# Optimization experiments

Hardware: AMD Instinct MI355X
Metric: run time of the kernel (lower is better)

The kernel has to match this reference:

```python
import math
import jax, jax.numpy as jnp
import numpy as np

G, PQ, PV = 12, 4, 8

def setup_inputs() -> dict:
    key = jax.random.key(0)
    ks = jax.random.split(key, 14)
    N, L, Cn, Ce, Ch = 1, 512, 384, 128, 192
    Node = jax.random.normal(ks[0], (N, L, Cn), jnp.float32)
    Edge = jax.random.normal(ks[1], (N, L, L, Ce), jnp.float32)
    # proper rotation matrices via QR of random gaussians
    raw = jax.random.normal(ks[2], (N, L, 3, 3), jnp.float32)
    rots, _ = jnp.linalg.qr(raw)
    trans = jax.random.normal(ks[3], (N, L, 3), jnp.float32) * 10.0
    def lin(k, fan_in, fan_out):
        return jax.random.normal(k, (fan_in, fan_out), jnp.float32) / np.sqrt(fan_in)
    return {
        'Node': Node, 'Edge': Edge, 'rots': rots, 'trans': trans,
        'Wq': lin(ks[4], Cn, Ch), 'Wk': lin(ks[5], Cn, Ch), 'Wv': lin(ks[6], Cn, Ch),
        'Wqv': lin(ks[7], Cn, 3 * G * PQ), 'Wkv': lin(ks[8], Cn, 3 * G * PQ),
        'Wvv': lin(ks[9], Cn, 3 * G * PV), 'Wbias': lin(ks[10], Ce, G),
        'gamma': jnp.zeros((G,), jnp.float32),
        'Wout': lin(ks[11], Ce * G + Ch + G * PV * 4, Cn),
        'bout': jnp.zeros((Cn,), jnp.float32),
    }

def reference(Node, Edge, rots, trans, Wq, Wk, Wv, Wqv, Wkv, Wvv, Wbias, gamma, Wout, bout):
    N, L, Cn = Node.shape
    Ce = Edge.shape[-1]
    Ch = Wq.shape[1]
    ppg = Ch // G
    t = trans / 10.0  # Frame(T.rots, T.trans / 10.0)
    q = (Node @ Wq).reshape(N, L, G, ppg)
    k = (Node @ Wk).reshape(N, L, G, ppg)
    v = (Node @ Wv).reshape(N, L, G, ppg)
    qv = (Node @ Wqv).reshape(N, L, G, PQ, 3)
    kv = (Node @ Wkv).reshape(N, L, G, PQ, 3)
    vv = (Node @ Wvv).reshape(N, L, G, PV, 3)
    apply_frame = lambda p: jnp.einsum('nlij,nlgpj->nlgpi', rots, p) + t[:, :, None, None]
    qv = apply_frame(qv)
    kv = apply_frame(kv)
    vv = apply_frame(vv)
    # pairwise squared point distances, summed over xyz and query points -> [N,L,L,G]
    d = qv[:, :, None] - kv[:, None]
    sq = jnp.sum(d * d, axis=(-1, -2))
    bias = jnp.einsum('nijc,cg->nijg', Edge, Wbias)
    WC = math.sqrt(2.0 / 9.0 / PQ)
    WL = math.sqrt(1.0 / 3.0)
    attn = jnp.einsum('nlgc,nmgc->nlmg', q, k) / math.sqrt(ppg) + bias
    attn = attn - jax.nn.softplus(gamma) * (WC / 2.0) * sq
    attn = jax.nn.softmax(WL * attn, axis=2)  # softmax over key index m
    O_Edge = jnp.einsum('nijg,nijc->nigc', attn, Edge).reshape(N, L, G * Ce)
    O_Node = jnp.einsum('nijg,njgc->nigc', attn, v).reshape(N, L, Ch)
    O_vec = jnp.einsum('nijg,njgpc->nigpc', attn, vv)
    # invert_apply: R^T (x - t)
    O_vec = jnp.einsum('nlji,nlgpj->nlgpi', rots, O_vec - t[:, :, None, None])
    O_norm = jnp.sqrt(jnp.sum(O_vec * O_vec, axis=-1) + 1e-8).reshape(N, L, -1)
    O_vec = O_vec.reshape(N, L, -1)
    feat = jnp.concatenate([O_Edge, O_Node, O_vec, O_norm], axis=-1)
    return feat @ Wout + bout
```

## Files before the change

kernel.cpp:

```cpp
#include <hip/hip_runtime.h>
#include <math.h>

#define LQ 512
#define CN 384
#define CE 128
#define CH 192
#define NG 12
#define PPG 16
#define FEAT 2112
#define NPROJ 1152

#define WS_RAW  0u
#define WS_QVG  589824u
#define WS_KVT  663552u
#define WS_VVG  737280u
#define WS_QN   884736u
#define WS_KNT  890880u
#define WS_KT   897024u
#define WS_ATT  995328u
#define WS_FEAT 4141056u
#define WS_PART 5222400u
#define WS_PM   WS_PART
#define WS_PS   (WS_PART + 12288u)

__global__ __launch_bounds__(256) void k1a_gemm(
    const float* __restrict__ Node,
    const float* __restrict__ Wq, const float* __restrict__ Wk,
    const float* __restrict__ Wv, const float* __restrict__ Wqv,
    const float* __restrict__ Wkv, const float* __restrict__ Wvv,
    float* __restrict__ ws)
{
    __shared__ float As[64][68];
    __shared__ float Bs[64][48];
    const int tid = threadIdx.x;
    const int cb = blockIdx.x % 24;
    const int l0 = (blockIdx.x / 24) * 64;
    const int col0 = cb * 48;

    const float* W; int nc, lc0;
    if (col0 < 192)      { W = Wq;  nc = 192; lc0 = col0; }
    else if (col0 < 384) { W = Wk;  nc = 192; lc0 = col0 - 192; }
    else if (col0 < 576) { W = Wv;  nc = 192; lc0 = col0 - 384; }
    else if (col0 < 720) { W = Wqv; nc = 144; lc0 = col0 - 576; }
    else if (col0 < 864) { W = Wkv; nc = 144; lc0 = col0 - 720; }
    else                 { W = Wvv; nc = 288; lc0 = col0 - 864; }

    const int tx = tid & 15, ty = tid >> 4;
    float acc[4][3];
#pragma unroll
    for (int r = 0; r < 4; ++r)
#pragma unroll
        for (int c = 0; c < 3; ++c) acc[r][c] = 0.f;

    for (int kc = 0; kc < 6; ++kc) {
        __syncthreads();
#pragma unroll
        for (int pass = 0; pass < 4; ++pass) {
            int m = (tid >> 4) + pass * 16;
            int kk = (tid & 15) * 4;
            const float4 a = *(const float4*)(Node + (size_t)(l0 + m) * CN + kc * 64 + kk);
            As[kk + 0][m] = a.x; As[kk + 1][m] = a.y;
            As[kk + 2][m] = a.z; As[kk + 3][m] = a.w;
        }
#pragma unroll
        for (int p = 0; p < 12; ++p) {
            int idx = p * 256 + tid;
            int kk = idx / 48, c = idx - kk * 48;
            Bs[kk][c] = W[(size_t)(kc * 64 + kk) * nc + lc0 + c];
        }
        __syncthreads();
#pragma unroll 8
        for (int kk = 0; kk < 64; ++kk) {
            const float4 av = *(const float4*)&As[kk][tx * 4];
            const float b0 = Bs[kk][ty * 3 + 0];
            const float b1 = Bs[kk][ty * 3 + 1];
            const float b2 = Bs[kk][ty * 3 + 2];
            acc[0][0] = fmaf(av.x, b0, acc[0][0]); acc[0][1] = fmaf(av.x, b1, acc[0][1]); acc[0][2] = fmaf(av.x, b2, acc[0][2]);
            acc[1][0] = fmaf(av.y, b0, acc[1][0]); acc[1][1] = fmaf(av.y, b1, acc[1][1]); acc[1][2] = fmaf(av.y, b2, acc[1][2]);
            acc[2][0] = fmaf(av.z, b0, acc[2][0]); acc[2][1] = fmaf(av.z, b1, acc[2][1]); acc[2][2] = fmaf(av.z, b2, acc[2][2]);
            acc[3][0] = fmaf(av.w, b0, acc[3][0]); acc[3][1] = fmaf(av.w, b1, acc[3][1]); acc[3][2] = fmaf(av.w, b2, acc[3][2]);
        }
    }
    float* raw = ws + WS_RAW;
#pragma unroll
    for (int r = 0; r < 4; ++r)
#pragma unroll
        for (int c = 0; c < 3; ++c)
            raw[(size_t)(l0 + tx * 4 + r) * NPROJ + col0 + ty * 3 + c] = acc[r][c];
    if (col0 >= 192 && col0 < 384) {
#pragma unroll
        for (int r = 0; r < 4; ++r)
#pragma unroll
            for (int c = 0; c < 3; ++c)
                ws[WS_KT + (size_t)(col0 - 192 + ty * 3 + c) * LQ + l0 + tx * 4 + r] = acc[r][c];
    }
}

__global__ __launch_bounds__(256) void k1b_vec(
    const float* __restrict__ rots, const float* __restrict__ trans,
    float* __restrict__ ws)
{
    __shared__ float sqbuf[96];
    const int tid = threadIdx.x;
    const int l = blockIdx.x;
    const float* raw = ws + WS_RAW + (size_t)l * NPROJ;

    if (tid < 192) {
        int src, pt, typ;
        if (tid < 48)      { typ = 0; pt = tid;      src = 576 + pt * 3; }
        else if (tid < 96) { typ = 1; pt = tid - 48; src = 720 + pt * 3; }
        else               { typ = 2; pt = tid - 96; src = 864 + pt * 3; }
        float v0 = raw[src], v1 = raw[src + 1], v2 = raw[src + 2];
        const float* R = rots + l * 9;
        float o0 = R[0] * v0 + R[1] * v1 + R[2] * v2 + trans[l * 3 + 0] * 0.1f;
        float o1 = R[3] * v0 + R[4] * v1 + R[5] * v2 + trans[l * 3 + 1] * 0.1f;
        float o2 = R[6] * v0 + R[7] * v1 + R[8] * v2 + trans[l * 3 + 2] * 0.1f;
        if (typ == 0) {
            float* dst = ws + WS_QVG + (size_t)l * 144 + pt * 3;
            dst[0] = o0; dst[1] = o1; dst[2] = o2;
        } else if (typ == 1) {
            ws[WS_KVT + (size_t)(pt * 3 + 0) * LQ + l] = o0;
            ws[WS_KVT + (size_t)(pt * 3 + 1) * LQ + l] = o1;
            ws[WS_KVT + (size_t)(pt * 3 + 2) * LQ + l] = o2;
        } else {
            float* dst = ws + WS_VVG + (size_t)l * 288 + pt * 3;
            dst[0] = o0; dst[1] = o1; dst[2] = o2;
        }
        if (tid < 96) sqbuf[tid] = o0 * o0 + o1 * o1 + o2 * o2;
    }
    __syncthreads();
    if (tid < 24) {
        int typ = tid / 12, g = tid % 12;
        int b = typ * 48 + g * 4;
        float s = sqbuf[b] + sqbuf[b + 1] + sqbuf[b + 2] + sqbuf[b + 3];
        if (typ == 0) ws[WS_QN + (size_t)l * 12 + g] = s;
        else          ws[WS_KNT + (size_t)g * LQ + l] = s;
    }
}

__global__ __launch_bounds__(256, 4) void k2_attn(
    const float* __restrict__ Edge, const float* __restrict__ Wbias,
    const float* __restrict__ gamma, float* __restrict__ ws)
{
    __shared__ float et[256 * 33];
    __shared__ float cgls[NG];
    __shared__ float red[4][NG];
    const int tid = threadIdx.x;
    const int i = blockIdx.x >> 1;
    const int h = blockIdx.x & 1;
    const int j = h * 256 + tid;

    if (tid < NG)
        cgls[tid] = log1pf(__expf(gamma[tid])) * 0.11785113019775793f;
    __syncthreads();

    float lgs[NG];
    {
        const float* qrow  = ws + WS_RAW + (size_t)i * NPROJ;
        const float* qvrow = ws + WS_QVG + (size_t)i * 144;
        const float* qnrow = ws + WS_QN  + (size_t)i * NG;
        const float* KT  = ws + WS_KT;
        const float* KVT = ws + WS_KVT;
        const float* KNT = ws + WS_KNT;
#pragma unroll
        for (int g = 0; g < NG; ++g) {
            float qk = 0.f;
#pragma unroll
            for (int u = 0; u < PPG; ++u)
                qk = fmaf(qrow[g * PPG + u], KT[(size_t)(g * PPG + u) * LQ + j], qk);
            float dt = 0.f;
#pragma unroll
            for (int u = 0; u < 12; ++u)
                dt = fmaf(qvrow[g * 12 + u], KVT[(size_t)(g * 12 + u) * LQ + j], dt);
            float sq = qnrow[g] + KNT[(size_t)g * LQ + j] - 2.f * dt;
            lgs[g] = qk * 0.25f - cgls[g] * sq;
        }
    }

    const float4* e4 = (const float4*)Edge + ((size_t)i * LQ + h * 256) * 32;
    for (int ch = 0; ch < 4; ++ch) {
        __syncthreads();
#pragma unroll
        for (int kk = 0; kk < 8; ++kk) {
            int idx = kk * 256 + tid;
            int jr = idx >> 3, c4 = idx & 7;
            float4 v = e4[(size_t)jr * 32 + ch * 8 + c4];
            float* d = et + jr * 33 + c4 * 4;
            d[0] = v.x; d[1] = v.y; d[2] = v.z; d[3] = v.w;
        }
        __syncthreads();
        const float* wbch = Wbias + ch * 32 * NG;
        const float* r0 = et + tid * 33;
#pragma unroll 4
        for (int c = 0; c < 32; ++c) {
            float e0 = r0[c];
            const float* wb = wbch + c * NG;
#pragma unroll
            for (int g = 0; g < NG; ++g) lgs[g] = fmaf(e0, wb[g], lgs[g]);
        }
    }

    const float WL = 0.5773502691896258f;
    const int wid = tid >> 6, lane = tid & 63;
    float pm[NG];
#pragma unroll
    for (int g = 0; g < NG; ++g) pm[g] = lgs[g];
#pragma unroll
    for (int g = 0; g < NG; ++g)
        for (int off = 1; off < 64; off <<= 1)
            pm[g] = fmaxf(pm[g], __shfl_xor(pm[g], off));
    if (lane == 0) {
#pragma unroll
        for (int g = 0; g < NG; ++g) red[wid][g] = pm[g];
    }
    __syncthreads();
    float gm[NG];
#pragma unroll
    for (int g = 0; g < NG; ++g)
        gm[g] = fmaxf(fmaxf(red[0][g], red[1][g]), fmaxf(red[2][g], red[3][g]));
    if (tid < NG)
        ws[WS_PM + ((size_t)i * 2 + h) * NG + tid] =
            fmaxf(fmaxf(red[0][tid], red[1][tid]), fmaxf(red[2][tid], red[3][tid]));
    __syncthreads();

    float ps[NG];
#pragma unroll
    for (int g = 0; g < NG; ++g) {
        float e = __expf(WL * (lgs[g] - gm[g]));
        lgs[g] = e;
        ps[g] = e;
    }
#pragma unroll
    for (int g = 0; g < NG; ++g)
        for (int off = 1; off < 64; off <<= 1)
            ps[g] += __shfl_xor(ps[g], off);
    if (lane == 0) {
#pragma unroll
        for (int g = 0; g < NG; ++g) red[wid][g] = ps[g];
    }
    __syncthreads();
    if (tid < NG)
        ws[WS_PS + ((size_t)i * 2 + h) * NG + tid] =
            red[0][tid] + red[1][tid] + red[2][tid] + red[3][tid];

    float4* dst = (float4*)(ws + WS_ATT + ((size_t)i * LQ + j) * NG);
    float4 s0, s1, s2;
    s0.x = lgs[0]; s0.y = lgs[1]; s0.z = lgs[2];  s0.w = lgs[3];
    s1.x = lgs[4]; s1.y = lgs[5]; s1.z = lgs[6];  s1.w = lgs[7];
    s2.x = lgs[8]; s2.y = lgs[9]; s2.z = lgs[10]; s2.w = lgs[11];
    dst[0] = s0; dst[1] = s1; dst[2] = s2;
}

__global__ __launch_bounds__(256) void k3_out(
    const float* __restrict__ Edge, const float* __restrict__ rots,
    const float* __restrict__ trans, float* __restrict__ ws)
{
    __shared__ float at[LQ][13];
    __shared__ float bufA[4][32][NG][4];
    __shared__ float ovec[288];
    __shared__ float sc[2][NG];
    const int tid = threadIdx.x;
    const int qi = blockIdx.x;
    const float* att = ws + WS_ATT + (size_t)qi * LQ * NG;

    if (tid < 24) {
        const float WL = 0.5773502691896258f;
        int hh = tid / NG, g = tid % NG;
        float m0 = ws[WS_PM + ((size_t)qi * 2 + 0) * NG + g];
        float m1 = ws[WS_PM + ((size_t)qi * 2 + 1) * NG + g];
        float ss0 = ws[WS_PS + ((size_t)qi * 2 + 0) * NG + g];
        float ss1 = ws[WS_PS + ((size_t)qi * 2 + 1) * NG + g];
        float m = fmaxf(m0, m1);
        float e0 = __expf(WL * (m0 - m));
        float e1 = __expf(WL * (m1 - m));
        float denom = ss0 * e0 + ss1 * e1;
        sc[hh][g] = (hh ? e1 : e0) / denom;
    }
    __syncthreads();

    for (int m = 0; m < 2; ++m) {
        int j = tid + m * 256;
        int hh = j >> 8;
        const float4* src = (const float4*)(att + (size_t)j * NG);
        float4 a = src[0], b = src[1], c = src[2];
        at[j][0] = a.x * sc[hh][0]; at[j][1] = a.y * sc[hh][1];
        at[j][2] = a.z * sc[hh][2]; at[j][3] = a.w * sc[hh][3];
        at[j][4] = b.x * sc[hh][4]; at[j][5] = b.y * sc[hh][5];
        at[j][6] = b.z * sc[hh][6]; at[j][7] = b.w * sc[hh][7];
        at[j][8] = c.x * sc[hh][8]; at[j][9] = c.y * sc[hh][9];
        at[j][10] = c.z * sc[hh][10]; at[j][11] = c.w * sc[hh][11];
    }
    __syncthreads();

    const int w = tid >> 6, lane = tid & 63, jh = lane >> 5, c4 = lane & 31;
    float acc[NG][4];
#pragma unroll
    for (int g = 0; g < NG; ++g)
#pragma unroll
        for (int r = 0; r < 4; ++r) acc[g][r] = 0.f;
    const float4* e4 = (const float4*)(Edge + (size_t)qi * LQ * CE);
    for (int jj = 0; jj < 64; ++jj) {
        int j = w * 128 + jh * 64 + jj;
        float4 e = e4[(size_t)j * 32 + c4];
#pragma unroll
        for (int g = 0; g < NG; ++g) {
            float a = at[j][g];
            acc[g][0] = fmaf(a, e.x, acc[g][0]);
            acc[g][1] = fmaf(a, e.y, acc[g][1]);
            acc[g][2] = fmaf(a, e.z, acc[g][2]);
            acc[g][3] = fmaf(a, e.w, acc[g][3]);
        }
    }
#pragma unroll
    for (int g = 0; g < NG; ++g)
#pragma unroll
        for (int r = 0; r < 4; ++r) acc[g][r] += __shfl_xor(acc[g][r], 32);
    if (jh == 0) {
#pragma unroll
        for (int g = 0; g < NG; ++g)
#pragma unroll
            for (int r = 0; r < 4; ++r) bufA[w][c4][g][r] = acc[g][r];
    }
    __syncthreads();
    float* feat = ws + WS_FEAT + (size_t)qi * FEAT;
    for (int m = 0; m < 6; ++m) {
        int o = tid + m * 256;
        int g = o >> 7, c = o & 127;
        int cc4 = c >> 2, r = c & 3;
        feat[o] = bufA[0][cc4][g][r] + bufA[1][cc4][g][r] +
                  bufA[2][cc4][g][r] + bufA[3][cc4][g][r];
    }

    const float* raw = ws + WS_RAW;
    const float* vvg = ws + WS_VVG;
    for (int ph = 0; ph < 2; ++ph) {
        int task = tid + ph * 256;
        if (task < 192) {
            int g = task >> 4;
            float s = 0.f;
            for (int j = 0; j < LQ; ++j) s = fmaf(at[j][g], raw[(size_t)j * NPROJ + 384 + task], s);
            feat[1536 + task] = s;
        } else if (task < 480) {
            int u = task - 192;
            int g = u / 24;
            float s = 0.f;
            for (int j = 0; j < LQ; ++j) s = fmaf(at[j][g], vvg[(size_t)j * 288 + u], s);
            ovec[u] = s;
        }
    }
    __syncthreads();

    if (tid < 96) {
        int g = tid >> 3, p = tid & 7;
        const float* R = rots + qi * 9;
        float t0 = trans[qi * 3 + 0] * 0.1f;
        float t1 = trans[qi * 3 + 1] * 0.1f;
        float t2 = trans[qi * 3 + 2] * 0.1f;
        float d0 = ovec[g * 24 + p * 3 + 0] - t0;
        float d1 = ovec[g * 24 + p * 3 + 1] - t1;
        float d2 = ovec[g * 24 + p * 3 + 2] - t2;
        float o0 = R[0] * d0 + R[3] * d1 + R[6] * d2;
        float o1 = R[1] * d0 + R[4] * d1 + R[7] * d2;
        float o2 = R[2] * d0 + R[5] * d1 + R[8] * d2;
        feat[1728 + g * 24 + p * 3 + 0] = o0;
        feat[1728 + g * 24 + p * 3 + 1] = o1;
        feat[1728 + g * 24 + p * 3 + 2] = o2;
        feat[2016 + g * 8 + p] = sqrtf(o0 * o0 + o1 * o1 + o2 * o2 + 1e-8f);
    }
}

__global__ __launch_bounds__(256) void k4_gemm(const float* __restrict__ Wout,
                                               float* __restrict__ ws)
{
    __shared__ float As[64][68];
    __shared__ float Bs[64][48];
    const int tid = threadIdx.x;
    const int cc = blockIdx.x >> 6;
    const int t  = blockIdx.x & 63;
    const int l0 = (t >> 3) * 64;
    const int col0 = (t & 7) * 48;
    const float* feat = ws + WS_FEAT;

    const int tx = tid & 15, ty = tid >> 4;
    float acc[4][3];
#pragma unroll
    for (int r = 0; r < 4; ++r)
#pragma unroll
        for (int c = 0; c < 3; ++c) acc[r][c] = 0.f;

    for (int kc = cc * 11; kc < cc * 11 + 11; ++kc) {
        __syncthreads();
#pragma unroll
        for (int pass = 0; pass < 4; ++pass) {
            int m = (tid >> 4) + pass * 16;
            int kk = (tid & 15) * 4;
            const float4 a = *(const float4*)(feat + (size_t)(l0 + m) * FEAT + kc * 64 + kk);
            As[kk + 0][m] = a.x; As[kk + 1][m] = a.y;
            As[kk + 2][m] = a.z; As[kk + 3][m] = a.w;
        }
#pragma unroll
        for (int p = 0; p < 12; ++p) {
            int idx = p * 256 + tid;
            int kk = idx / 48, c = idx - kk * 48;
            Bs[kk][c] = Wout[(size_t)(kc * 64 + kk) * CN + col0 + c];
        }
        __syncthreads();
#pragma unroll 8
        for (int kk = 0; kk < 64; ++kk) {
            const float4 av = *(const float4*)&As[kk][tx * 4];
            const float b0 = Bs[kk][ty * 3 + 0];
            const float b1 = Bs[kk][ty * 3 + 1];
            const float b2 = Bs[kk][ty * 3 + 2];
            acc[0][0] = fmaf(av.x, b0, acc[0][0]); acc[0][1] = fmaf(av.x, b1, acc[0][1]); acc[0][2] = fmaf(av.x, b2, acc[0][2]);
            acc[1][0] = fmaf(av.y, b0, acc[1][0]); acc[1][1] = fmaf(av.y, b1, acc[1][1]); acc[1][2] = fmaf(av.y, b2, acc[1][2]);
            acc[2][0] = fmaf(av.z, b0, acc[2][0]); acc[2][1] = fmaf(av.z, b1, acc[2][1]); acc[2][2] = fmaf(av.z, b2, acc[2][2]);
            acc[3][0] = fmaf(av.w, b0, acc[3][0]); acc[3][1] = fmaf(av.w, b1, acc[3][1]); acc[3][2] = fmaf(av.w, b2, acc[3][2]);
        }
    }
    float* part = ws + WS_PART + (size_t)cc * LQ * CN;
#pragma unroll
    for (int r = 0; r < 4; ++r)
#pragma unroll
        for (int c = 0; c < 3; ++c)
            part[(size_t)(l0 + tx * 4 + r) * CN + col0 + ty * 3 + c] = acc[r][c];
}

__global__ __launch_bounds__(384) void k5_red(const float* __restrict__ bout,
                                              const float* __restrict__ wsc,
                                              float* __restrict__ out)
{
    const int i = blockIdx.x, n = threadIdx.x;
    const float* part = wsc + WS_PART;
    size_t idx = (size_t)i * CN + n;
    size_t st = (size_t)LQ * CN;
    out[idx] = part[idx] + part[st + idx] + part[2 * st + idx] + bout[n];
}

extern "C" void kernel_launch(void* const* d_in, const int* in_sizes, int n_in,
                              void* d_out, int out_size, void* d_ws, size_t ws_size,
                              hipStream_t stream) {
    const float* Node  = (const float*)d_in[0];
    const float* Edge  = (const float*)d_in[1];
    const float* rots  = (const float*)d_in[2];
    const float* trans = (const float*)d_in[3];
    const float* Wq    = (const float*)d_in[4];
    const float* Wk    = (const float*)d_in[5];
    const float* Wv    = (const float*)d_in[6];
    const float* Wqv   = (const float*)d_in[7];
    const float* Wkv   = (const float*)d_in[8];
    const float* Wvv   = (const float*)d_in[9];
    const float* Wbias = (const float*)d_in[10];
    const float* gamma = (const float*)d_in[11];
    const float* Wout  = (const float*)d_in[12];
    const float* bout  = (const float*)d_in[13];
    float* ws = (float*)d_ws;

    k1a_gemm<<<192, 256, 0, stream>>>(Node, Wq, Wk, Wv, Wqv, Wkv, Wvv, ws);
    k1b_vec<<<512, 256, 0, stream>>>(rots, trans, ws);
    k2_attn<<<1024, 256, 0, stream>>>(Edge, Wbias, gamma, ws);
    k3_out<<<512, 256, 0, stream>>>(Edge, rots, trans, ws);
    k4_gemm<<<192, 256, 0, stream>>>(Wout, ws);
    k5_red<<<512, 384, 0, stream>>>(bout, ws, (float*)d_out);
}
```

Measured before the change: 202.0 us.

## Fuse attention-weighted Edge reduction into attention kernel to avoid second Edge read

Computes per-half partial O_Edge sums inside k2 using the unnormalized exponentials kept in shared memory, and stores them to workspace. k3 then combines the two halves with the softmax rescale factors instead of rereading Edge. This removes a second full pass over the large Edge tensor. In exchange k2 uses more shared memory, lowers its occupancy bound, and re-streams Edge chunks through shared memory.

```diff
diff --git a/kernel.cpp b/kernel.cpp
--- a/kernel.cpp
+++ b/kernel.cpp
@@ -22,6 +22,7 @@
 #define WS_PART 5222400u
 #define WS_PM   WS_PART
 #define WS_PS   (WS_PART + 12288u)
+#define WS_OEP  5812224u
 
 __global__ __launch_bounds__(256) void k1a_gemm(
     const float* __restrict__ Node,
@@ -138,11 +139,12 @@
     }
 }
 
-__global__ __launch_bounds__(256, 4) void k2_attn(
+__global__ __launch_bounds__(256, 3) void k2_attn(
     const float* __restrict__ Edge, const float* __restrict__ Wbias,
     const float* __restrict__ gamma, float* __restrict__ ws)
 {
     __shared__ float et[256 * 33];
+    __shared__ float exl[256 * 13];
     __shared__ float cgls[NG];
     __shared__ float red[4][NG];
     const int tid = threadIdx.x;
@@ -229,6 +231,7 @@
         float e = __expf(WL * (lgs[g] - gm[g]));
         lgs[g] = e;
         ps[g] = e;
+        exl[tid * 13 + g] = e;
     }
 #pragma unroll
     for (int g = 0; g < NG; ++g)
@@ -243,20 +246,72 @@
         ws[WS_PS + ((size_t)i * 2 + h) * NG + tid] =
             red[0][tid] + red[1][tid] + red[2][tid] + red[3][tid];
 
-    float4* dst = (float4*)(ws + WS_ATT + ((size_t)i * LQ + j) * NG);
-    float4 s0, s1, s2;
-    s0.x = lgs[0]; s0.y = lgs[1]; s0.z = lgs[2];  s0.w = lgs[3];
-    s1.x = lgs[4]; s1.y = lgs[5]; s1.z = lgs[6];  s1.w = lgs[7];
-    s2.x = lgs[8]; s2.y = lgs[9]; s2.z = lgs[10]; s2.w = lgs[11];
-    dst[0] = s0; dst[1] = s1; dst[2] = s2;
+    {
+        float4* dst = (float4*)(ws + WS_ATT + ((size_t)i * LQ + j) * NG);
+        float4 s0, s1, s2;
+        s0.x = lgs[0]; s0.y = lgs[1]; s0.z = lgs[2];  s0.w = lgs[3];
+        s1.x = lgs[4]; s1.y = lgs[5]; s1.z = lgs[6];  s1.w = lgs[7];
+        s2.x = lgs[8]; s2.y = lgs[9]; s2.z = lgs[10]; s2.w = lgs[11];
+        dst[0] = s0; dst[1] = s1; dst[2] = s2;
+    }
+
+    const int jsub = lane >> 3, c4f = lane & 7;
+    const int g0 = wid * 3;
+    float* oep = ws + WS_OEP + ((size_t)i * 2 + h) * (NG * CE);
+    for (int ch = 0; ch < 4; ++ch) {
+        __syncthreads();
+#pragma unroll
+        for (int kk = 0; kk < 8; ++kk) {
+            int idx = kk * 256 + tid;
+            int jr = idx >> 3, c4 = idx & 7;
+            float4 v = e4[(size_t)jr * 32 + ch * 8 + c4];
+            float* d = et + jr * 33 + c4 * 4;
+            d[0] = v.x; d[1] = v.y; d[2] = v.z; d[3] = v.w;
+        }
+        __syncthreads();
+        float acc[3][4];
+#pragma unroll
+        for (int a = 0; a < 3; ++a)
+#pragma unroll
+            for (int r = 0; r < 4; ++r) acc[a][r] = 0.f;
+#pragma unroll 4
+        for (int jj = 0; jj < 32; ++jj) {
+            int jr = jj * 8 + jsub;
+            const float* er = et + jr * 33 + c4f * 4;
+            float e0 = er[0], e1 = er[1], e2 = er[2], e3 = er[3];
+            const float* ex = exl + jr * 13 + g0;
+#pragma unroll
+            for (int a = 0; a < 3; ++a) {
+                float aa = ex[a];
+                acc[a][0] = fmaf(aa, e0, acc[a][0]);
+                acc[a][1] = fmaf(aa, e1, acc[a][1]);
+                acc[a][2] = fmaf(aa, e2, acc[a][2]);
+                acc[a][3] = fmaf(aa, e3, acc[a][3]);
+            }
+        }
+#pragma unroll
+        for (int a = 0; a < 3; ++a)
+#pragma unroll
+            for (int r = 0; r < 4; ++r) {
+                acc[a][r] += __shfl_xor(acc[a][r], 8);
+                acc[a][r] += __shfl_xor(acc[a][r], 16);
+                acc[a][r] += __shfl_xor(acc[a][r], 32);
+            }
+        if (jsub == 0) {
+#pragma unroll
+            for (int a = 0; a < 3; ++a)
+#pragma unroll
+                for (int r = 0; r < 4; ++r)
+                    oep[(g0 + a) * CE + ch * 32 + c4f * 4 + r] = acc[a][r];
+        }
+    }
 }
 
 __global__ __launch_bounds__(256) void k3_out(
-    const float* __restrict__ Edge, const float* __restrict__ rots,
-    const float* __restrict__ trans, float* __restrict__ ws)
+    const float* __restrict__ rots, const float* __restrict__ trans,
+    float* __restrict__ ws)
 {
     __shared__ float at[LQ][13];
-    __shared__ float bufA[4][32][NG][4];
     __shared__ float ovec[288];
     __shared__ float sc[2][NG];
     const int tid = threadIdx.x;
@@ -278,6 +333,17 @@
     }
     __syncthreads();
 
+    float* feat = ws + WS_FEAT + (size_t)qi * FEAT;
+    {
+        const float* oep0 = ws + WS_OEP + ((size_t)qi * 2 + 0) * (NG * CE);
+        const float* oep1 = ws + WS_OEP + ((size_t)qi * 2 + 1) * (NG * CE);
+        for (int m = 0; m < 6; ++m) {
+            int o = tid + m * 256;
+            int g = o >> 7;
+            feat[o] = sc[0][g] * oep0[o] + sc[1][g] * oep1[o];
+        }
+    }
+
     for (int m = 0; m < 2; ++m) {
         int j = tid + m * 256;
         int hh = j >> 8;
@@ -291,45 +357,6 @@
         at[j][10] = c.z * sc[hh][10]; at[j][11] = c.w * sc[hh][11];
     }
     __syncthreads();
-
-    const int w = tid >> 6, lane = tid & 63, jh = lane >> 5, c4 = lane & 31;
-    float acc[NG][4];
-#pragma unroll
-    for (int g = 0; g < NG; ++g)
-#pragma unroll
-        for (int r = 0; r < 4; ++r) acc[g][r] = 0.f;
-    const float4* e4 = (const float4*)(Edge + (size_t)qi * LQ * CE);
-    for (int jj = 0; jj < 64; ++jj) {
-        int j = w * 128 + jh * 64 + jj;
-        float4 e = e4[(size_t)j * 32 + c4];
-#pragma unroll
-        for (int g = 0; g < NG; ++g) {
-            float a = at[j][g];
-            acc[g][0] = fmaf(a, e.x, acc[g][0]);
-            acc[g][1] = fmaf(a, e.y, acc[g][1]);
-            acc[g][2] = fmaf(a, e.z, acc[g][2]);
-            acc[g][3] = fmaf(a, e.w, acc[g][3]);
-        }
-    }
-#pragma unroll
-    for (int g = 0; g < NG; ++g)
-#pragma unroll
-        for (int r = 0; r < 4; ++r) acc[g][r] += __shfl_xor(acc[g][r], 32);
-    if (jh == 0) {
-#pragma unroll
-        for (int g = 0; g < NG; ++g)
-#pragma unroll
-            for (int r = 0; r < 4; ++r) bufA[w][c4][g][r] = acc[g][r];
-    }
-    __syncthreads();
-    float* feat = ws + WS_FEAT + (size_t)qi * FEAT;
-    for (int m = 0; m < 6; ++m) {
-        int o = tid + m * 256;
-        int g = o >> 7, c = o & 127;
-        int cc4 = c >> 2, r = c & 3;
-        feat[o] = bufA[0][cc4][g][r] + bufA[1][cc4][g][r] +
-                  bufA[2][cc4][g][r] + bufA[3][cc4][g][r];
-    }
 
     const float* raw = ws + WS_RAW;
     const float* vvg = ws + WS_VVG;
@@ -458,7 +485,7 @@
     k1a_gemm<<<192, 256, 0, stream>>>(Node, Wq, Wk, Wv, Wqv, Wkv, Wvv, ws);
     k1b_vec<<<512, 256, 0, stream>>>(rots, trans, ws);
     k2_attn<<<1024, 256, 0, stream>>>(Edge, Wbias, gamma, ws);
-    k3_out<<<512, 256, 0, stream>>>(Edge, rots, trans, ws);
+    k3_out<<<512, 256, 0, stream>>>(rots, trans, ws);
     k4_gemm<<<192, 256, 0, stream>>>(Wout, ws);
     k5_red<<<512, 384, 0, stream>>>(bout, ws, (float*)d_out);
 }
```

Result: slower. 213.7 us (+5.8%).

## Fuse edge bias, softmax exponentials and edge aggregation into single Edge pass

Applied to the files above, without the earlier changes.

Splits the attention kernel into a logits kernel and an edge kernel that streams each Edge row once. In that one pass it computes the bias, the unnormalised softmax weights, the partial sums and the partial O_Edge accumulations, which removes the second full read of the large Edge tensor in the output kernel. The softmax no longer subtracts the running max, which saves the reduction passes but risks overflow or underflow for large logits. It adds workspace traffic for partial O_Edge and sum buffers, and the output kernel is split across two blocks per query.

```diff
diff --git a/kernel.cpp b/kernel.cpp
--- a/kernel.cpp
+++ b/kernel.cpp
@@ -9,6 +9,7 @@
 #define PPG 16
 #define FEAT 2112
 #define NPROJ 1152
+#define WLs 0.5773502691896258f
 
 #define WS_RAW  0u
 #define WS_QVG  589824u
@@ -20,8 +21,9 @@
 #define WS_ATT  995328u
 #define WS_FEAT 4141056u
 #define WS_PART 5222400u
-#define WS_PM   WS_PART
-#define WS_PS   (WS_PART + 12288u)
+#define WS_PS2  5812224u
+#define WS_LGS  5861376u
+#define WS_OEP  9007104u
 
 __global__ __launch_bounds__(256) void k1a_gemm(
     const float* __restrict__ Node,
@@ -138,13 +140,10 @@
     }
 }
 
-__global__ __launch_bounds__(256, 4) void k2_attn(
-    const float* __restrict__ Edge, const float* __restrict__ Wbias,
+__global__ __launch_bounds__(256) void k2a_logits(
     const float* __restrict__ gamma, float* __restrict__ ws)
 {
-    __shared__ float et[256 * 33];
     __shared__ float cgls[NG];
-    __shared__ float red[4][NG];
     const int tid = threadIdx.x;
     const int i = blockIdx.x >> 1;
     const int h = blockIdx.x & 1;
@@ -154,96 +153,27 @@
         cgls[tid] = log1pf(__expf(gamma[tid])) * 0.11785113019775793f;
     __syncthreads();
 
+    const float* qrow  = ws + WS_RAW + (size_t)i * NPROJ;
+    const float* qvrow = ws + WS_QVG + (size_t)i * 144;
+    const float* qnrow = ws + WS_QN  + (size_t)i * NG;
+    const float* KT  = ws + WS_KT;
+    const float* KVT = ws + WS_KVT;
+    const float* KNT = ws + WS_KNT;
     float lgs[NG];
-    {
-        const float* qrow  = ws + WS_RAW + (size_t)i * NPROJ;
-        const float* qvrow = ws + WS_QVG + (size_t)i * 144;
-        const float* qnrow = ws + WS_QN  + (size_t)i * NG;
-        const float* KT  = ws + WS_KT;
-        const float* KVT = ws + WS_KVT;
-        const float* KNT = ws + WS_KNT;
-#pragma unroll
-        for (int g = 0; g < NG; ++g) {
-            float qk = 0.f;
-#pragma unroll
-            for (int u = 0; u < PPG; ++u)
-                qk = fmaf(qrow[g * PPG + u], KT[(size_t)(g * PPG + u) * LQ + j], qk);
-            float dt = 0.f;
-#pragma unroll
-            for (int u = 0; u < 12; ++u)
-                dt = fmaf(qvrow[g * 12 + u], KVT[(size_t)(g * 12 + u) * LQ + j], dt);
-            float sq = qnrow[g] + KNT[(size_t)g * LQ + j] - 2.f * dt;
-            lgs[g] = qk * 0.25f - cgls[g] * sq;
-        }
-    }
-
-    const float4* e4 = (const float4*)Edge + ((size_t)i * LQ + h * 256) * 32;
-    for (int ch = 0; ch < 4; ++ch) {
-        __syncthreads();
-#pragma unroll
-        for (int kk = 0; kk < 8; ++kk) {
-            int idx = kk * 256 + tid;
-            int jr = idx >> 3, c4 = idx & 7;
-            float4 v = e4[(size_t)jr * 32 + ch * 8 + c4];
-            float* d = et + jr * 33 + c4 * 4;
-            d[0] = v.x; d[1] = v.y; d[2] = v.z; d[3] = v.w;
-        }
-        __syncthreads();
-        const float* wbch = Wbias + ch * 32 * NG;
-        const float* r0 = et + tid * 33;
-#pragma unroll 4
-        for (int c = 0; c < 32; ++c) {
-            float e0 = r0[c];
-            const float* wb = wbch + c * NG;
-#pragma unroll
-            for (int g = 0; g < NG; ++g) lgs[g] = fmaf(e0, wb[g], lgs[g]);
-        }
-    }
-
-    const float WL = 0.5773502691896258f;
-    const int wid = tid >> 6, lane = tid & 63;
-    float pm[NG];
-#pragma unroll
-    for (int g = 0; g < NG; ++g) pm[g] = lgs[g];
-#pragma unroll
-    for (int g = 0; g < NG; ++g)
-        for (int off = 1; off < 64; off <<= 1)
-            pm[g] = fmaxf(pm[g], __shfl_xor(pm[g], off));
-    if (lane == 0) {
-#pragma unroll
-        for (int g = 0; g < NG; ++g) red[wid][g] = pm[g];
-    }
-    __syncthreads();
-    float gm[NG];
-#pragma unroll
-    for (int g = 0; g < NG; ++g)
-        gm[g] = fmaxf(fmaxf(red[0][g], red[1][g]), fmaxf(red[2][g], red[3][g]));
-    if (tid < NG)
-        ws[WS_PM + ((size_t)i * 2 + h) * NG + tid] =
-            fmaxf(fmaxf(red[0][tid], red[1][tid]), fmaxf(red[2][tid], red[3][tid]));
-    __syncthreads();
-
-    float ps[NG];
 #pragma unroll
     for (int g = 0; g < NG; ++g) {
-        float e = __expf(WL * (lgs[g] - gm[g]));
-        lgs[g] = e;
-        ps[g] = e;
-    }
-#pragma unroll
-    for (int g = 0; g < NG; ++g)
-        for (int off = 1; off < 64; off <<= 1)
-            ps[g] += __shfl_xor(ps[g], off);
-    if (lane == 0) {
-#pragma unroll
-        for (int g = 0; g < NG; ++g) red[wid][g] = ps[g];
-    }
-    __syncthreads();
-    if (tid < NG)
-        ws[WS_PS + ((size_t)i * 2 + h) * NG + tid] =
-            red[0][tid] + red[1][tid] + red[2][tid] + red[3][tid];
-
-    float4* dst = (float4*)(ws + WS_ATT + ((size_t)i * LQ + j) * NG);
+        float qk = 0.f;
+#pragma unroll
+        for (int u = 0; u < PPG; ++u)
+            qk = fmaf(qrow[g * PPG + u], KT[(size_t)(g * PPG + u) * LQ + j], qk);
+        float dt = 0.f;
+#pragma unroll
+        for (int u = 0; u < 12; ++u)
+            dt = fmaf(qvrow[g * 12 + u], KVT[(size_t)(g * 12 + u) * LQ + j], dt);
+        float sq = qnrow[g] + KNT[(size_t)g * LQ + j] - 2.f * dt;
+        lgs[g] = qk * 0.25f - cgls[g] * sq;
+    }
+    float4* dst = (float4*)(ws + WS_LGS + ((size_t)i * LQ + j) * NG);
     float4 s0, s1, s2;
     s0.x = lgs[0]; s0.y = lgs[1]; s0.z = lgs[2];  s0.w = lgs[3];
     s1.x = lgs[4]; s1.y = lgs[5]; s1.z = lgs[6];  s1.w = lgs[7];
@@ -251,121 +181,194 @@
     dst[0] = s0; dst[1] = s1; dst[2] = s2;
 }
 
-__global__ __launch_bounds__(256) void k3_out(
-    const float* __restrict__ Edge, const float* __restrict__ rots,
-    const float* __restrict__ trans, float* __restrict__ ws)
+__global__ __launch_bounds__(256) void k2b_edge(
+    const float* __restrict__ Edge, const float* __restrict__ Wbias,
+    float* __restrict__ ws)
+{
+    const int tid = threadIdx.x;
+    const int i = blockIdx.x >> 1;
+    const int h = blockIdx.x & 1;
+    const int w = tid >> 6, lane = tid & 63;
+    const int half = lane >> 5, c4 = lane & 31;
+    const int j0 = h * 256 + w * 64;
+
+    float wb[4][NG];
+#pragma unroll
+    for (int r = 0; r < 4; ++r)
+#pragma unroll
+        for (int g = 0; g < NG; ++g)
+            wb[r][g] = Wbias[(c4 * 4 + r) * NG + g];
+
+    float oea[NG][4];
+#pragma unroll
+    for (int g = 0; g < NG; ++g)
+#pragma unroll
+        for (int r = 0; r < 4; ++r) oea[g][r] = 0.f;
+    float ps[NG];
+#pragma unroll
+    for (int g = 0; g < NG; ++g) ps[g] = 0.f;
+
+    const float* ebase = Edge + ((size_t)i * LQ + j0) * CE;
+    const float* lgsb  = ws + WS_LGS + ((size_t)i * LQ + j0) * NG;
+    float* attb        = ws + WS_ATT + ((size_t)i * LQ + j0) * NG;
+
+    float4 cur = *(const float4*)(ebase + (size_t)half * CE + c4 * 4);
+    for (int p = 0; p < 32; ++p) {
+        float4 nxt;
+        if (p < 31)
+            nxt = *(const float4*)(ebase + (size_t)(2 * p + 2 + half) * CE + c4 * 4);
+        float b[NG];
+#pragma unroll
+        for (int g = 0; g < NG; ++g)
+            b[g] = fmaf(cur.x, wb[0][g], fmaf(cur.y, wb[1][g],
+                   fmaf(cur.z, wb[2][g], cur.w * wb[3][g])));
+#pragma unroll
+        for (int off = 1; off < 32; off <<= 1)
+#pragma unroll
+            for (int g = 0; g < NG; ++g) b[g] += __shfl_xor(b[g], off);
+        const float4* lg4 = (const float4*)(lgsb + (size_t)(2 * p + half) * NG);
+        float4 L0 = lg4[0], L1 = lg4[1], L2 = lg4[2];
+        float e[NG];
+        e[0] = __expf(WLs * (b[0] + L0.x)); e[1] = __expf(WLs * (b[1] + L0.y));
+        e[2] = __expf(WLs * (b[2] + L0.z)); e[3] = __expf(WLs * (b[3] + L0.w));
+        e[4] = __expf(WLs * (b[4] + L1.x)); e[5] = __expf(WLs * (b[5] + L1.y));
+        e[6] = __expf(WLs * (b[6] + L1.z)); e[7] = __expf(WLs * (b[7] + L1.w));
+        e[8] = __expf(WLs * (b[8] + L2.x)); e[9] = __expf(WLs * (b[9] + L2.y));
+        e[10] = __expf(WLs * (b[10] + L2.z)); e[11] = __expf(WLs * (b[11] + L2.w));
+#pragma unroll
+        for (int g = 0; g < NG; ++g) {
+            ps[g] += e[g];
+            oea[g][0] = fmaf(e[g], cur.x, oea[g][0]);
+            oea[g][1] = fmaf(e[g], cur.y, oea[g][1]);
+            oea[g][2] = fmaf(e[g], cur.z, oea[g][2]);
+            oea[g][3] = fmaf(e[g], cur.w, oea[g][3]);
+        }
+        if (c4 == 0) {
+            float4 s0, s1, s2;
+            s0.x = e[0]; s0.y = e[1]; s0.z = e[2];  s0.w = e[3];
+            s1.x = e[4]; s1.y = e[5]; s1.z = e[6];  s1.w = e[7];
+            s2.x = e[8]; s2.y = e[9]; s2.z = e[10]; s2.w = e[11];
+            float4* d = (float4*)(attb + (size_t)(2 * p + half) * NG);
+            d[0] = s0; d[1] = s1; d[2] = s2;
+        }
+        cur = nxt;
+    }
+#pragma unroll
+    for (int g = 0; g < NG; ++g) {
+        ps[g] += __shfl_xor(ps[g], 32);
+#pragma unroll
+        for (int r = 0; r < 4; ++r) oea[g][r] += __shfl_xor(oea[g][r], 32);
+    }
+    const int wslot = h * 4 + w;
+    if (lane == 0) {
+        float* d = ws + WS_PS2 + ((size_t)i * 8 + wslot) * NG;
+        float4 s0, s1, s2;
+        s0.x = ps[0]; s0.y = ps[1]; s0.z = ps[2];  s0.w = ps[3];
+        s1.x = ps[4]; s1.y = ps[5]; s1.z = ps[6];  s1.w = ps[7];
+        s2.x = ps[8]; s2.y = ps[9]; s2.z = ps[10]; s2.w = ps[11];
+        ((float4*)d)[0] = s0; ((float4*)d)[1] = s1; ((float4*)d)[2] = s2;
+    }
+    if (half == 0) {
+        float* ob = ws + WS_OEP + ((size_t)(i * 8 + wslot) * NG) * CE;
+#pragma unroll
+        for (int g = 0; g < NG; ++g) {
+            float4 v;
+            v.x = oea[g][0]; v.y = oea[g][1]; v.z = oea[g][2]; v.w = oea[g][3];
+            *(float4*)(ob + (size_t)g * CE + c4 * 4) = v;
+        }
+    }
+}
+
+__global__ __launch_bounds__(256) void k3b_out(
+    const float* __restrict__ rots, const float* __restrict__ trans,
+    float* __restrict__ ws)
 {
     __shared__ float at[LQ][13];
-    __shared__ float bufA[4][32][NG][4];
-    __shared__ float ovec[288];
-    __shared__ float sc[2][NG];
-    const int tid = threadIdx.x;
-    const int qi = blockIdx.x;
+    __shared__ float invl[NG];
+    __shared__ float ovecl[240];
+    const int tid = threadIdx.x;
+    const int qi = blockIdx.x >> 1;
+    const int s  = blockIdx.x & 1;
+
+    if (tid < NG) {
+        float t = 0.f;
+        for (int w = 0; w < 8; ++w)
+            t += ws[WS_PS2 + ((size_t)qi * 8 + w) * NG + tid];
+        invl[tid] = 1.f / t;
+    }
+    __syncthreads();
+    float inv[NG];
+#pragma unroll
+    for (int g = 0; g < NG; ++g) inv[g] = invl[g];
+
     const float* att = ws + WS_ATT + (size_t)qi * LQ * NG;
-
-    if (tid < 24) {
-        const float WL = 0.5773502691896258f;
-        int hh = tid / NG, g = tid % NG;
-        float m0 = ws[WS_PM + ((size_t)qi * 2 + 0) * NG + g];
-        float m1 = ws[WS_PM + ((size_t)qi * 2 + 1) * NG + g];
-        float ss0 = ws[WS_PS + ((size_t)qi * 2 + 0) * NG + g];
-        float ss1 = ws[WS_PS + ((size_t)qi * 2 + 1) * NG + g];
-        float m = fmaxf(m0, m1);
-        float e0 = __expf(WL * (m0 - m));
-        float e1 = __expf(WL * (m1 - m));
-        float denom = ss0 * e0 + ss1 * e1;
-        sc[hh][g] = (hh ? e1 : e0) / denom;
-    }
-    __syncthreads();
-
     for (int m = 0; m < 2; ++m) {
         int j = tid + m * 256;
-        int hh = j >> 8;
         const float4* src = (const float4*)(att + (size_t)j * NG);
         float4 a = src[0], b = src[1], c = src[2];
-        at[j][0] = a.x * sc[hh][0]; at[j][1] = a.y * sc[hh][1];
-        at[j][2] = a.z * sc[hh][2]; at[j][3] = a.w * sc[hh][3];
-        at[j][4] = b.x * sc[hh][4]; at[j][5] = b.y * sc[hh][5];
-        at[j][6] = b.z * sc[hh][6]; at[j][7] = b.w * sc[hh][7];
-        at[j][8] = c.x * sc[hh][8]; at[j][9] = c.y * sc[hh][9];
-        at[j][10] = c.z * sc[hh][10]; at[j][11] = c.w * sc[hh][11];
+        at[j][0] = a.x * inv[0]; at[j][1] = a.y * inv[1];
+        at[j][2] = a.z * inv[2]; at[j][3] = a.w * inv[3];
+        at[j][4] = b.x * inv[4]; at[j][5] = b.y * inv[5];
+        at[j][6] = b.z * inv[6]; at[j][7] = b.w * inv[7];
+        at[j][8] = c.x * inv[8]; at[j][9] = c.y * inv[9];
+        at[j][10] = c.z * inv[10]; at[j][11] = c.w * inv[11];
+    }
+
+    float* feat = ws + WS_FEAT + (size_t)qi * FEAT;
+    {
+        const float* ob = ws + WS_OEP + (size_t)qi * 8 * NG * CE;
+#pragma unroll
+        for (int m = 0; m < 3; ++m) {
+            int o = s * 768 + m * 256 + tid;
+            float t = 0.f;
+#pragma unroll
+            for (int w = 0; w < 8; ++w) t += ob[(size_t)w * NG * CE + o];
+            feat[o] = t * inv[o >> 7];
+        }
     }
     __syncthreads();
-
-    const int w = tid >> 6, lane = tid & 63, jh = lane >> 5, c4 = lane & 31;
-    float acc[NG][4];
-#pragma unroll
-    for (int g = 0; g < NG; ++g)
-#pragma unroll
-        for (int r = 0; r < 4; ++r) acc[g][r] = 0.f;
-    const float4* e4 = (const float4*)(Edge + (size_t)qi * LQ * CE);
-    for (int jj = 0; jj < 64; ++jj) {
-        int j = w * 128 + jh * 64 + jj;
-        float4 e = e4[(size_t)j * 32 + c4];
-#pragma unroll
-        for (int g = 0; g < NG; ++g) {
-            float a = at[j][g];
-            acc[g][0] = fmaf(a, e.x, acc[g][0]);
-            acc[g][1] = fmaf(a, e.y, acc[g][1]);
-            acc[g][2] = fmaf(a, e.z, acc[g][2]);
-            acc[g][3] = fmaf(a, e.w, acc[g][3]);
-        }
-    }
-#pragma unroll
-    for (int g = 0; g < NG; ++g)
-#pragma unroll
-        for (int r = 0; r < 4; ++r) acc[g][r] += __shfl_xor(acc[g][r], 32);
-    if (jh == 0) {
-#pragma unroll
-        for (int g = 0; g < NG; ++g)
-#pragma unroll
-            for (int r = 0; r < 4; ++r) bufA[w][c4][g][r] = acc[g][r];
-    }
-    __syncthreads();
-    float* feat = ws + WS_FEAT + (size_t)qi * FEAT;
-    for (int m = 0; m < 6; ++m) {
-        int o = tid + m * 256;
-        int g = o >> 7, c = o & 127;
-        int cc4 = c >> 2, r = c & 3;
-        feat[o] = bufA[0][cc4][g][r] + bufA[1][cc4][g][r] +
-                  bufA[2][cc4][g][r] + bufA[3][cc4][g][r];
-    }
 
     const float* raw = ws + WS_RAW;
     const float* vvg = ws + WS_VVG;
-    for (int ph = 0; ph < 2; ++ph) {
-        int task = tid + ph * 256;
-        if (task < 192) {
-            int g = task >> 4;
-            float s = 0.f;
-            for (int j = 0; j < LQ; ++j) s = fmaf(at[j][g], raw[(size_t)j * NPROJ + 384 + task], s);
-            feat[1536 + task] = s;
-        } else if (task < 480) {
-            int u = task - 192;
+    if (tid < 240) {
+        if (s == 0 && tid < 192) {
+            int g = tid >> 4;
+            float sum = 0.f;
+#pragma unroll 4
+            for (int j = 0; j < LQ; ++j)
+                sum = fmaf(at[j][g], raw[(size_t)j * NPROJ + 384 + tid], sum);
+            feat[1536 + tid] = sum;
+        } else {
+            int u = (s == 0) ? (tid - 192) : (48 + tid);
+            int lidx = (s == 0) ? (tid - 192) : tid;
             int g = u / 24;
-            float s = 0.f;
-            for (int j = 0; j < LQ; ++j) s = fmaf(at[j][g], vvg[(size_t)j * 288 + u], s);
-            ovec[u] = s;
+            float sum = 0.f;
+#pragma unroll 4
+            for (int j = 0; j < LQ; ++j)
+                sum = fmaf(at[j][g], vvg[(size_t)j * 288 + u], sum);
+            ovecl[lidx] = sum;
         }
     }
     __syncthreads();
 
-    if (tid < 96) {
-        int g = tid >> 3, p = tid & 7;
+    int npts = (s == 0) ? 16 : 80;
+    if (tid < npts) {
+        int P = (s == 0) ? tid : (16 + tid);
+        int u0l = (s == 0) ? (P * 3) : (P * 3 - 48);
         const float* R = rots + qi * 9;
         float t0 = trans[qi * 3 + 0] * 0.1f;
         float t1 = trans[qi * 3 + 1] * 0.1f;
         float t2 = trans[qi * 3 + 2] * 0.1f;
-        float d0 = ovec[g * 24 + p * 3 + 0] - t0;
-        float d1 = ovec[g * 24 + p * 3 + 1] - t1;
-        float d2 = ovec[g * 24 + p * 3 + 2] - t2;
+        float d0 = ovecl[u0l + 0] - t0;
+        float d1 = ovecl[u0l + 1] - t1;
+        float d2 = ovecl[u0l + 2] - t2;
         float o0 = R[0] * d0 + R[3] * d1 + R[6] * d2;
         float o1 = R[1] * d0 + R[4] * d1 + R[7] * d2;
         float o2 = R[2] * d0 + R[5] * d1 + R[8] * d2;
-        feat[1728 + g * 24 + p * 3 + 0] = o0;
-        feat[1728 + g * 24 + p * 3 + 1] = o1;
-        feat[1728 + g * 24 + p * 3 + 2] = o2;
-        feat[2016 + g * 8 + p] = sqrtf(o0 * o0 + o1 * o1 + o2 * o2 + 1e-8f);
+        feat[1728 + P * 3 + 0] = o0;
+        feat[1728 + P * 3 + 1] = o1;
+        feat[1728 + P * 3 + 2] = o2;
+        feat[2016 + P] = sqrtf(o0 * o0 + o1 * o1 + o2 * o2 + 1e-8f);
     }
 }
 
@@ -457,8 +460,9 @@
 
     k1a_gemm<<<192, 256, 0, stream>>>(Node, Wq, Wk, Wv, Wqv, Wkv, Wvv, ws);
     k1b_vec<<<512, 256, 0, stream>>>(rots, trans, ws);
-    k2_attn<<<1024, 256, 0, stream>>>(Edge, Wbias, gamma, ws);
-    k3_out<<<512, 256, 0, stream>>>(Edge, rots, trans, ws);
+    k2a_logits<<<1024, 256, 0, stream>>>(gamma, ws);
+    k2b_edge<<<1024, 256, 0, stream>>>(Edge, Wbias, ws);
+    k3b_out<<<1024, 256, 0, stream>>>(rots, trans, ws);
     k4_gemm<<<192, 256, 0, stream>>>(Wout, ws);
     k5_red<<<512, 384, 0, stream>>>(bout, ws, (float*)d_out);
 }
```

Result: slower. 261.3 us (+29.4%).
